# Kernel optimization log

Measured on AMD Instinct MI355X. Metric: run time of the kernel, lower is better.

Reference implementation:

```python
import jax, jax.numpy as jnp
import numpy as np
import math

THETA = 10000.0

def _rope(x, pos):
    # x: [B, H, S, Dh], pos: [S]
    d = x.shape[-1]
    inv_freq = 1.0 / (THETA ** (jnp.arange(0, d, 2, dtype=jnp.float32) / d))  # [Dh/2]
    ang = pos.astype(jnp.float32)[:, None] * inv_freq[None, :]                # [S, Dh/2]
    cos, sin = jnp.cos(ang), jnp.sin(ang)
    x1, x2 = x[..., 0::2], x[..., 1::2]
    r1 = x1 * cos - x2 * sin
    r2 = x1 * sin + x2 * cos
    return jnp.stack([r1, r2], axis=-1).reshape(x.shape)

def setup_inputs() -> dict:
    key = jax.random.key(0)
    ks = jax.random.split(key, 5)
    B, S, D = 2, 1024, 2048
    Dkv = 512
    scale = 1.0 / math.sqrt(D)
    return {
        "X": jax.random.normal(ks[0], (B, S, D), dtype=jnp.float32),
        "token_positions": jnp.arange(S, dtype=jnp.int32),
        "q_w": jax.random.normal(ks[1], (D, D), dtype=jnp.float32) * scale,
        "k_w": jax.random.normal(ks[2], (Dkv, D), dtype=jnp.float32) * scale,
        "v_w": jax.random.normal(ks[3], (Dkv, D), dtype=jnp.float32) * scale,
        "o_w": jax.random.normal(ks[4], (D, D), dtype=jnp.float32) * scale,
    }

def reference(X, token_positions, q_w, k_w, v_w, o_w):
    B, S, D = X.shape
    H, Hkv = 32, 8
    Dh = D // H
    G = H // Hkv  # query heads per KV head

    Q = (X @ q_w.T).reshape(B, S, H, Dh).transpose(0, 2, 1, 3)      # [B,H,S,Dh]
    K = (X @ k_w.T).reshape(B, S, Hkv, Dh).transpose(0, 2, 1, 3)    # [B,Hkv,S,Dh]
    V = (X @ v_w.T).reshape(B, S, Hkv, Dh).transpose(0, 2, 1, 3)    # [B,Hkv,S,Dh]

    Q = _rope(Q, token_positions)
    K = _rope(K, token_positions)

    # group query heads: [B, Hkv, G, S, Dh]
    Qg = Q.reshape(B, Hkv, G, S, Dh)
    scores = jnp.einsum('bkgqd,bkld->bkgql', Qg, K) / math.sqrt(Dh)  # [B,Hkv,G,S,S]
    causal = jnp.tril(jnp.ones((S, S), dtype=bool))
    scores = jnp.where(causal, scores, -jnp.inf)
    probs = jax.nn.softmax(scores, axis=-1)
    attn = jnp.einsum('bkgql,bkld->bkgqd', probs, V)                 # [B,Hkv,G,S,Dh]

    attn = attn.reshape(B, H, S, Dh).transpose(0, 2, 1, 3).reshape(B, S, D)
    return attn @ o_w.T
```

## Files before the change

### kernel.cpp

```cpp
#include <hip/hip_runtime.h>

typedef _Float16 f16;
typedef _Float16 half8 __attribute__((ext_vector_type(8), may_alias));
typedef _Float16 half4 __attribute__((ext_vector_type(4), may_alias));
typedef float f32x4 __attribute__((ext_vector_type(4), may_alias));

#define ROPE_KF -0.41524101186092027f
#define QSCALE 0.18033688011112042f

__device__ __forceinline__ void gload_lds16(const f16* g, f16* lds) {
  __builtin_amdgcn_global_load_lds(
      (const __attribute__((address_space(1))) void*)g,
      (__attribute__((address_space(3))) void*)lds, 16, 0, 0);
}

template <int N>
__device__ __forceinline__ void vm_wait() {
  if constexpr (N == 0) asm volatile("s_waitcnt vmcnt(0)" ::: "memory");
  else if constexpr (N == 3) asm volatile("s_waitcnt vmcnt(3)" ::: "memory");
  else if constexpr (N == 4) asm volatile("s_waitcnt vmcnt(4)" ::: "memory");
}

__device__ __forceinline__ half8 rope8s(half8 va, half8 vb, float posf, int i0,
                                        float scale) {
  half8 r;
#pragma unroll
  for (int p = 0; p < 4; ++p) {
    const float ang = posf * exp2f(ROPE_KF * (float)(i0 + p));
    float s, c;
    sincosf(ang, &s, &c);
    const float x1 = (float)va[2 * p] + (float)vb[2 * p];
    const float x2 = (float)va[2 * p + 1] + (float)vb[2 * p + 1];
    r[2 * p]     = (f16)((x1 * c - x2 * s) * scale);
    r[2 * p + 1] = (f16)((x1 * s + x2 * c) * scale);
  }
  return r;
}

__global__ __launch_bounds__(256) void cvt_all(const float* __restrict__ s0, f16* __restrict__ d0, int n0,
                                               const float* __restrict__ s1, f16* __restrict__ d1, int n1,
                                               const float* __restrict__ s2, f16* __restrict__ d2, int n2,
                                               const float* __restrict__ s3, f16* __restrict__ d3, int n3,
                                               const float* __restrict__ s4, f16* __restrict__ d4, int n4) {
  const int step = gridDim.x * blockDim.x * 4;
  const int base = (blockIdx.x * blockDim.x + threadIdx.x) * 4;
  auto go = [&](const float* s, f16* d, int n) {
    for (int i = base; i < n; i += step) {
      float4 v = *(const float4*)(s + i);
      half4 h;
      h[0] = (f16)v.x; h[1] = (f16)v.y; h[2] = (f16)v.z; h[3] = (f16)v.w;
      *(half4*)(d + i) = h;
    }
  };
  go(s0, d0, n0); go(s1, d1, n1); go(s2, d2, n2); go(s3, d3, n3); go(s4, d4, n4);
}

template <int OUT_F32, int BM>
__global__ __launch_bounds__(256, 2) void gemm_bt(const f16* __restrict__ A,
                                                  const f16* __restrict__ B,
                                                  void* __restrict__ Cv,
                                                  int M, int N, int K) {
  constexpr int NJ = (BM == 128) ? 4 : 2;
  constexpr int ACH = BM / 64;
  constexpr int LPS = ACH + 2;

  __shared__ alignas(16) f16 As[2][BM][32];
  __shared__ alignas(16) f16 Bs[2][128][32];
  const int tid = threadIdx.x;
  const int w = tid >> 6, l = tid & 63;
  const int m0 = blockIdx.y * BM, n0 = blockIdx.x << 7;
  const int klen = K / gridDim.z;
  const int koff = blockIdx.z * klen;
  const int fr = l & 15;
  const int fkz = (((l >> 4) ^ ((fr >> 1) & 3)) << 3);
  const int wr = (BM == 128) ? ((w >> 1) << 6) : 0;
  const int wc = (BM == 128) ? ((w & 1) << 6) : (w << 5);
  const int srow = l >> 2;
  const int scol = (((l & 3) ^ ((l >> 3) & 3)) << 3);

  const f16* ga = A + (size_t)(m0 + srow) * K + koff + scol;
  const f16* gb = B + (size_t)(n0 + srow) * K + koff + scol;

  auto stage = [&](int buf, int t) {
    const int k0 = t << 5;
#pragma unroll
    for (int c = 0; c < ACH; ++c) {
      const int rb = (w * ACH + c) << 4;
      gload_lds16(ga + (size_t)rb * K + k0, &As[buf][rb][0]);
    }
#pragma unroll
    for (int c = 0; c < 2; ++c) {
      const int rb = (w * 2 + c) << 4;
      gload_lds16(gb + (size_t)rb * K + k0, &Bs[buf][rb][0]);
    }
  };

  f32x4 acc[4][NJ] = {};

  stage(0, 0);
  stage(1, 1);
  const int nk = klen >> 5;
  for (int t = 0; t < nk; ++t) {
    const int buf = t & 1;
    if (t + 1 < nk) vm_wait<LPS>();
    else vm_wait<0>();
    __builtin_amdgcn_s_barrier();
    __builtin_amdgcn_sched_barrier(0);
    half8 af[4], bf[NJ];
#pragma unroll
    for (int i = 0; i < 4; ++i) af[i] = *(const half8*)&As[buf][wr + i * 16 + fr][fkz];
#pragma unroll
    for (int j = 0; j < NJ; ++j) bf[j] = *(const half8*)&Bs[buf][wc + j * 16 + fr][fkz];
#pragma unroll
    for (int i = 0; i < 4; ++i)
#pragma unroll
      for (int j = 0; j < NJ; ++j)
        acc[i][j] = __builtin_amdgcn_mfma_f32_16x16x32_f16(af[i], bf[j], acc[i][j], 0, 0, 0);
    __builtin_amdgcn_sched_barrier(0);
    __builtin_amdgcn_s_barrier();
    if (t + 2 < nk) stage(buf, t + 2);
  }

  const size_t zoff = (size_t)blockIdx.z * M * (size_t)N;
  const int orow = (l >> 4) << 2;
#pragma unroll
  for (int i = 0; i < 4; ++i) {
#pragma unroll
    for (int j = 0; j < NJ; ++j) {
      const int col = n0 + wc + j * 16 + fr;
#pragma unroll
      for (int r = 0; r < 4; ++r) {
        const size_t idx = zoff + (size_t)(m0 + wr + i * 16 + orow + r) * N + col;
        if (OUT_F32) ((float*)Cv)[idx] = acc[i][j][r];
        else ((f16*)Cv)[idx] = (f16)acc[i][j][r];
      }
    }
  }
}

__global__ __launch_bounds__(256) void repack_kv(const f16* __restrict__ QKV0,
                                                 const f16* __restrict__ QKV1,
                                                 const int* __restrict__ pos,
                                                 f16* __restrict__ Kp,
                                                 f16* __restrict__ Vt) {
  const int kt = blockIdx.x, kvh = blockIdx.y, b = blockIdx.z;
  const int tid = threadIdx.x;
  __shared__ f16 vs[64][72];
  const size_t tile = ((size_t)((b * 8 + kvh) * 16 + kt)) * 4096;
  const size_t kcol = 2048 + kvh * 64, vcol = 2560 + kvh * 64;
#pragma unroll
  for (int p = 0; p < 2; ++p) {
    const int c = tid + p * 256;
    const int row = c >> 3, slot = c & 7;
    const size_t grow = (size_t)(b * 1024 + kt * 64 + row) * 3072 + slot * 8;
    const half8 k0 = *(const half8*)(QKV0 + grow + kcol);
    const half8 k1 = *(const half8*)(QKV1 + grow + kcol);
    const half8 kk = rope8s(k0, k1, (float)pos[kt * 64 + row], slot << 2, 1.0f);
    *(half8*)(Kp + tile + row * 64 + ((slot ^ (row & 7)) << 3)) = kk;
    const half8 v0 = *(const half8*)(QKV0 + grow + vcol);
    const half8 v1 = *(const half8*)(QKV1 + grow + vcol);
    half8 vv;
#pragma unroll
    for (int ii = 0; ii < 8; ++ii) vv[ii] = (f16)((float)v0[ii] + (float)v1[ii]);
    *(half8*)&vs[row][slot * 8] = vv;
  }
  __syncthreads();
#pragma unroll
  for (int p = 0; p < 2; ++p) {
    const int c = tid + p * 256;
    const int d = c >> 3, oct = c & 7;
    half8 vv;
#pragma unroll
    for (int m = 0; m < 8; ++m) vv[m] = vs[oct * 8 + m][d];
    *(half8*)(Vt + tile + d * 64 + ((oct ^ (d & 7)) << 3)) = vv;
  }
}

__global__ __launch_bounds__(256) void attn_fwd(const f16* __restrict__ QKV0,
                                                const f16* __restrict__ QKV1,
                                                const f16* __restrict__ Kp,
                                                const f16* __restrict__ Vt,
                                                const int* __restrict__ pos,
                                                f16* __restrict__ O) {
  const int flat = blockIdx.x + (blockIdx.y << 3) + (blockIdx.z << 8);
  const int rmid = ((flat & 7) << 6) + (flat >> 3);
  const int pr = rmid & 7, h = (rmid >> 3) & 31, b = rmid >> 8;
  const int kvh = h >> 2;
  const int tid = threadIdx.x, w = tid >> 6, l = tid & 63;
  const int fr = l & 15, g = l >> 4;
  const int orow = g << 2;
  const int qtA = pr, qtB = 15 - pr;

  __shared__ alignas(16) char KsB[2][8192];
  __shared__ alignas(16) char VtB[2][8192];
  __shared__ alignas(16) f16 Ps[4][16][72];

  auto KS = [&](int buf, int row, int slot) -> f16* {
    return (f16*)(KsB[buf] + row * 128 + ((slot ^ (row & 7)) << 4));
  };
  auto VT = [&](int buf, int d, int oct) -> f16* {
    return (f16*)(VtB[buf] + d * 128 + ((oct ^ (d & 7)) << 4));
  };

  const int sA = qtA * 64 + w * 16 + fr, sB = qtB * 64 + w * 16 + fr;
  const float pA = (float)pos[sA], pB = (float)pos[sB];
  const size_t qoff = (size_t)(b * 1024 + w * 16 + fr) * 3072 + h * 64 + (g << 3);
  const size_t qoA = qoff + (size_t)qtA * 64 * 3072;
  const size_t qoB = qoff + (size_t)qtB * 64 * 3072;
  const half8 aA0 = rope8s(*(const half8*)(QKV0 + qoA), *(const half8*)(QKV1 + qoA),
                           pA, g << 2, QSCALE);
  const half8 aA1 = rope8s(*(const half8*)(QKV0 + qoA + 32), *(const half8*)(QKV1 + qoA + 32),
                           pA, 16 + (g << 2), QSCALE);
  const half8 aB0 = rope8s(*(const half8*)(QKV0 + qoB), *(const half8*)(QKV1 + qoB),
                           pB, g << 2, QSCALE);
  const half8 aB1 = rope8s(*(const half8*)(QKV0 + qoB + 32), *(const half8*)(QKV1 + qoB + 32),
                           pB, 16 + (g << 2), QSCALE);

  float rlA[4] = {0.f, 0.f, 0.f, 0.f}, rlB[4] = {0.f, 0.f, 0.f, 0.f};
  f32x4 oA[4] = {}, oB[4] = {};

  const size_t tbase = ((size_t)((b * 8 + kvh) * 16)) * 4096;
  const f16* kp0 = Kp + tbase + w * 1024 + (l << 3);
  const f16* vp0 = Vt + tbase + w * 1024 + (l << 3);
  auto stage = [&](int buf, int kt) {
    const f16* kp = kp0 + (size_t)kt * 4096;
    const f16* vp = vp0 + (size_t)kt * 4096;
    f16* kl = (f16*)(KsB[buf] + w * 2048);
    f16* vl = (f16*)(VtB[buf] + w * 2048);
    gload_lds16(kp, kl);
    gload_lds16(kp + 512, kl + 512);
    gload_lds16(vp, vl);
    gload_lds16(vp + 512, vl + 512);
  };

  auto compute = [&](int buf, const half8& a0, const half8& a1, float* rl,
                     f32x4* o, int qt, int kt) {
    f32x4 s4[4] = {};
#pragma unroll
    for (int j = 0; j < 4; ++j) {
      const half8 bk0 = *(const half8*)KS(buf, j * 16 + fr, g);
      const half8 bk1 = *(const half8*)KS(buf, j * 16 + fr, 4 + g);
      s4[j] = __builtin_amdgcn_mfma_f32_16x16x32_f16(a0, bk0, s4[j], 0, 0, 0);
      s4[j] = __builtin_amdgcn_mfma_f32_16x16x32_f16(a1, bk1, s4[j], 0, 0, 0);
    }
    if (kt == qt) {
      const int qrow0 = qt * 64 + w * 16 + orow;
#pragma unroll
      for (int j = 0; j < 4; ++j) {
        const int col = kt * 64 + j * 16 + fr;
#pragma unroll
        for (int r = 0; r < 4; ++r)
          if (col > qrow0 + r) s4[j][r] = -1.0e30f;
      }
    }
    float ps[4] = {0.f, 0.f, 0.f, 0.f};
#pragma unroll
    for (int j = 0; j < 4; ++j)
#pragma unroll
      for (int r = 0; r < 4; ++r) {
        const float p = exp2f(s4[j][r]);
        ps[r] += p;
        Ps[w][orow + r][j * 16 + fr] = (f16)p;
      }
#pragma unroll
    for (int r = 0; r < 4; ++r) rl[r] += ps[r];
#pragma unroll
    for (int kv2 = 0; kv2 < 2; ++kv2) {
      const half8 ap = *(const half8*)&Ps[w][fr][kv2 * 32 + (g << 3)];
#pragma unroll
      for (int j = 0; j < 4; ++j) {
        const half8 bv = *(const half8*)VT(buf, j * 16 + fr, kv2 * 4 + g);
        o[j] = __builtin_amdgcn_mfma_f32_16x16x32_f16(ap, bv, o[j], 0, 0, 0);
      }
    }
  };

  stage(0, 0);
  stage(1, 1);
  for (int kt = 0; kt <= qtB; ++kt) {
    const int buf = kt & 1;
    if (kt < qtB) vm_wait<4>();
    else vm_wait<0>();
    __builtin_amdgcn_s_barrier();
    __builtin_amdgcn_sched_barrier(0);
    if (kt <= qtA) compute(buf, aA0, aA1, rlA, oA, qtA, kt);
    compute(buf, aB0, aB1, rlB, oB, qtB, kt);
    __builtin_amdgcn_sched_barrier(0);
    __builtin_amdgcn_s_barrier();
    if (kt + 2 <= qtB) stage(buf, kt + 2);
  }

#pragma unroll
  for (int r = 0; r < 4; ++r) {
#pragma unroll
    for (int off = 8; off >= 1; off >>= 1) {
      rlA[r] += __shfl_xor(rlA[r], off);
      rlB[r] += __shfl_xor(rlB[r], off);
    }
  }

#pragma unroll
  for (int j = 0; j < 4; ++j)
#pragma unroll
    for (int r = 0; r < 4; ++r) {
      const int rowA = qtA * 64 + w * 16 + orow + r;
      const int rowB = qtB * 64 + w * 16 + orow + r;
      const int col = h * 64 + j * 16 + fr;
      O[(size_t)(b * 1024 + rowA) * 2048 + col] = (f16)(oA[j][r] / rlA[r]);
      O[(size_t)(b * 1024 + rowB) * 2048 + col] = (f16)(oB[j][r] / rlB[r]);
    }
}

extern "C" void kernel_launch(void* const* d_in, const int* in_sizes, int n_in,
                              void* d_out, int out_size, void* d_ws, size_t ws_size,
                              hipStream_t stream) {
  const float* X = (const float*)d_in[0];
  const int* tokpos = (const int*)d_in[1];
  const float* qw = (const float*)d_in[2];
  const float* kw = (const float*)d_in[3];
  const float* vw = (const float*)d_in[4];
  const float* ow = (const float*)d_in[5];

  constexpr int B = 2, S = 1024, D = 2048, DKV = 512, H = 32;
  constexpr int M = B * S;
  constexpr int NQKV = D + 2 * DKV;

  char* ws = (char*)d_ws;
  f16* Xh    = (f16*)(ws);
  f16* QKVW  = (f16*)(ws + (8u << 20));
  f16* owh   = (f16*)(ws + (20u << 20));
  f16* QKVc0 = (f16*)(ws + (28u << 20));
  f16* QKVc1 = (f16*)(ws + (40u << 20));
  f16* Kp    = (f16*)(ws);
  f16* Vt    = (f16*)(ws + (2u << 20));
  f16* Ah    = (f16*)(ws + (4u << 20));

  cvt_all<<<2048, 256, 0, stream>>>(X, Xh, M * D,
                                    qw, QKVW, D * D,
                                    kw, QKVW + (size_t)D * D, DKV * D,
                                    vw, QKVW + (size_t)(D + DKV) * D, DKV * D,
                                    ow, owh, D * D);

  gemm_bt<0, 128><<<dim3(NQKV / 128, M / 128, 2), 256, 0, stream>>>(Xh, QKVW, QKVc0,
                                                                    M, NQKV, D);

  repack_kv<<<dim3(16, 8, 2), 256, 0, stream>>>(QKVc0, QKVc1, tokpos, Kp, Vt);

  attn_fwd<<<dim3(8, H, B), 256, 0, stream>>>(QKVc0, QKVc1, Kp, Vt, tokpos, Ah);

  gemm_bt<1, 64><<<dim3(D / 128, M / 64, 1), 256, 0, stream>>>(Ah, owh, d_out, M, D, D);
}
```

Before: 121.4 us.

## Halve attention query tile per block and split-K the output projection

The attention kernel now runs 128-thread blocks over 32-row query tiles, each paired with its causal mirror, which doubles the block count to 1024. Each of the two waves loads twice as many K/V chunks per stage. The output projection switches to the 128-row split-K GEMM that writes two fp16 partial buffers, and a new reduce_out kernel sums them into fp32. The aim is better occupancy and load balance on the GPU. The cost is an extra kernel launch, an extra memory round trip, and partial sums rounded to fp16 before the final add.

```diff
diff --git a/kernel.cpp b/kernel.cpp
--- a/kernel.cpp
+++ b/kernel.cpp
@@ -19,6 +19,7 @@
   if constexpr (N == 0) asm volatile("s_waitcnt vmcnt(0)" ::: "memory");
   else if constexpr (N == 3) asm volatile("s_waitcnt vmcnt(3)" ::: "memory");
   else if constexpr (N == 4) asm volatile("s_waitcnt vmcnt(4)" ::: "memory");
+  else if constexpr (N == 8) asm volatile("s_waitcnt vmcnt(8)" ::: "memory");
 }
 
 __device__ __forceinline__ half8 rope8s(half8 va, half8 vb, float posf, int i0,
@@ -55,6 +56,23 @@
   go(s0, d0, n0); go(s1, d1, n1); go(s2, d2, n2); go(s3, d3, n3); go(s4, d4, n4);
 }
 
+__global__ __launch_bounds__(256) void reduce_out(const f16* __restrict__ a,
+                                                  const f16* __restrict__ b,
+                                                  float* __restrict__ o, int n) {
+  const int step = gridDim.x * blockDim.x * 8;
+  for (int i = (blockIdx.x * blockDim.x + threadIdx.x) * 8; i < n; i += step) {
+    const half8 va = *(const half8*)(a + i);
+    const half8 vb = *(const half8*)(b + i);
+    float4 o0, o1;
+    o0.x = (float)va[0] + (float)vb[0]; o0.y = (float)va[1] + (float)vb[1];
+    o0.z = (float)va[2] + (float)vb[2]; o0.w = (float)va[3] + (float)vb[3];
+    o1.x = (float)va[4] + (float)vb[4]; o1.y = (float)va[5] + (float)vb[5];
+    o1.z = (float)va[6] + (float)vb[6]; o1.w = (float)va[7] + (float)vb[7];
+    *(float4*)(o + i) = o0;
+    *(float4*)(o + i + 4) = o1;
+  }
+}
+
 template <int OUT_F32, int BM>
 __global__ __launch_bounds__(256, 2) void gemm_bt(const f16* __restrict__ A,
                                                   const f16* __restrict__ B,
@@ -176,24 +194,25 @@
   }
 }
 
-__global__ __launch_bounds__(256) void attn_fwd(const f16* __restrict__ QKV0,
+__global__ __launch_bounds__(128) void attn_fwd(const f16* __restrict__ QKV0,
                                                 const f16* __restrict__ QKV1,
                                                 const f16* __restrict__ Kp,
                                                 const f16* __restrict__ Vt,
                                                 const int* __restrict__ pos,
                                                 f16* __restrict__ O) {
-  const int flat = blockIdx.x + (blockIdx.y << 3) + (blockIdx.z << 8);
-  const int rmid = ((flat & 7) << 6) + (flat >> 3);
-  const int pr = rmid & 7, h = (rmid >> 3) & 31, b = rmid >> 8;
+  const int flat = blockIdx.x + (blockIdx.y << 4) + (blockIdx.z << 9);
+  const int rmid = ((flat & 7) << 7) + (flat >> 3);
+  const int pr = rmid & 15, h = (rmid >> 4) & 31, b = rmid >> 9;
   const int kvh = h >> 2;
   const int tid = threadIdx.x, w = tid >> 6, l = tid & 63;
   const int fr = l & 15, g = l >> 4;
   const int orow = g << 2;
-  const int qtA = pr, qtB = 15 - pr;
+  const int qtA = pr, qtB = 31 - pr;
+  const int ktA = qtA >> 1, ktB = qtB >> 1;
 
   __shared__ alignas(16) char KsB[2][8192];
   __shared__ alignas(16) char VtB[2][8192];
-  __shared__ alignas(16) f16 Ps[4][16][72];
+  __shared__ alignas(16) f16 Ps[2][16][72];
 
   auto KS = [&](int buf, int row, int slot) -> f16* {
     return (f16*)(KsB[buf] + row * 128 + ((slot ^ (row & 7)) << 4));
@@ -202,11 +221,11 @@
     return (f16*)(VtB[buf] + d * 128 + ((oct ^ (d & 7)) << 4));
   };
 
-  const int sA = qtA * 64 + w * 16 + fr, sB = qtB * 64 + w * 16 + fr;
+  const int sA = qtA * 32 + w * 16 + fr, sB = qtB * 32 + w * 16 + fr;
   const float pA = (float)pos[sA], pB = (float)pos[sB];
   const size_t qoff = (size_t)(b * 1024 + w * 16 + fr) * 3072 + h * 64 + (g << 3);
-  const size_t qoA = qoff + (size_t)qtA * 64 * 3072;
-  const size_t qoB = qoff + (size_t)qtB * 64 * 3072;
+  const size_t qoA = qoff + (size_t)qtA * 32 * 3072;
+  const size_t qoB = qoff + (size_t)qtB * 32 * 3072;
   const half8 aA0 = rope8s(*(const half8*)(QKV0 + qoA), *(const half8*)(QKV1 + qoA),
                            pA, g << 2, QSCALE);
   const half8 aA1 = rope8s(*(const half8*)(QKV0 + qoA + 32), *(const half8*)(QKV1 + qoA + 32),
@@ -220,17 +239,18 @@
   f32x4 oA[4] = {}, oB[4] = {};
 
   const size_t tbase = ((size_t)((b * 8 + kvh) * 16)) * 4096;
-  const f16* kp0 = Kp + tbase + w * 1024 + (l << 3);
-  const f16* vp0 = Vt + tbase + w * 1024 + (l << 3);
+  const f16* kp0 = Kp + tbase + w * 2048 + (l << 3);
+  const f16* vp0 = Vt + tbase + w * 2048 + (l << 3);
   auto stage = [&](int buf, int kt) {
     const f16* kp = kp0 + (size_t)kt * 4096;
     const f16* vp = vp0 + (size_t)kt * 4096;
-    f16* kl = (f16*)(KsB[buf] + w * 2048);
-    f16* vl = (f16*)(VtB[buf] + w * 2048);
-    gload_lds16(kp, kl);
-    gload_lds16(kp + 512, kl + 512);
-    gload_lds16(vp, vl);
-    gload_lds16(vp + 512, vl + 512);
+    f16* kl = (f16*)(KsB[buf] + w * 4096);
+    f16* vl = (f16*)(VtB[buf] + w * 4096);
+#pragma unroll
+    for (int c = 0; c < 4; ++c) {
+      gload_lds16(kp + c * 512, kl + c * 512);
+      gload_lds16(vp + c * 512, vl + c * 512);
+    }
   };
 
   auto compute = [&](int buf, const half8& a0, const half8& a1, float* rl,
@@ -243,8 +263,8 @@
       s4[j] = __builtin_amdgcn_mfma_f32_16x16x32_f16(a0, bk0, s4[j], 0, 0, 0);
       s4[j] = __builtin_amdgcn_mfma_f32_16x16x32_f16(a1, bk1, s4[j], 0, 0, 0);
     }
-    if (kt == qt) {
-      const int qrow0 = qt * 64 + w * 16 + orow;
+    if (kt == (qt >> 1)) {
+      const int qrow0 = qt * 32 + w * 16 + orow;
 #pragma unroll
       for (int j = 0; j < 4; ++j) {
         const int col = kt * 64 + j * 16 + fr;
@@ -277,17 +297,17 @@
 
   stage(0, 0);
   stage(1, 1);
-  for (int kt = 0; kt <= qtB; ++kt) {
+  for (int kt = 0; kt <= ktB; ++kt) {
     const int buf = kt & 1;
-    if (kt < qtB) vm_wait<4>();
+    if (kt < ktB) vm_wait<8>();
     else vm_wait<0>();
     __builtin_amdgcn_s_barrier();
     __builtin_amdgcn_sched_barrier(0);
-    if (kt <= qtA) compute(buf, aA0, aA1, rlA, oA, qtA, kt);
+    if (kt <= ktA) compute(buf, aA0, aA1, rlA, oA, qtA, kt);
     compute(buf, aB0, aB1, rlB, oB, qtB, kt);
     __builtin_amdgcn_sched_barrier(0);
     __builtin_amdgcn_s_barrier();
-    if (kt + 2 <= qtB) stage(buf, kt + 2);
+    if (kt + 2 <= ktB) stage(buf, kt + 2);
   }
 
 #pragma unroll
@@ -303,8 +323,8 @@
   for (int j = 0; j < 4; ++j)
 #pragma unroll
     for (int r = 0; r < 4; ++r) {
-      const int rowA = qtA * 64 + w * 16 + orow + r;
-      const int rowB = qtB * 64 + w * 16 + orow + r;
+      const int rowA = qtA * 32 + w * 16 + orow + r;
+      const int rowB = qtB * 32 + w * 16 + orow + r;
       const int col = h * 64 + j * 16 + fr;
       O[(size_t)(b * 1024 + rowA) * 2048 + col] = (f16)(oA[j][r] / rlA[r]);
       O[(size_t)(b * 1024 + rowB) * 2048 + col] = (f16)(oB[j][r] / rlB[r]);
@@ -334,6 +354,7 @@
   f16* Kp    = (f16*)(ws);
   f16* Vt    = (f16*)(ws + (2u << 20));
   f16* Ah    = (f16*)(ws + (4u << 20));
+  f16* Oh    = (f16*)(ws + (28u << 20));
 
   cvt_all<<<2048, 256, 0, stream>>>(X, Xh, M * D,
                                     qw, QKVW, D * D,
@@ -346,7 +367,9 @@
 
   repack_kv<<<dim3(16, 8, 2), 256, 0, stream>>>(QKVc0, QKVc1, tokpos, Kp, Vt);
 
-  attn_fwd<<<dim3(8, H, B), 256, 0, stream>>>(QKVc0, QKVc1, Kp, Vt, tokpos, Ah);
-
-  gemm_bt<1, 64><<<dim3(D / 128, M / 64, 1), 256, 0, stream>>>(Ah, owh, d_out, M, D, D);
-}
+  attn_fwd<<<dim3(16, H, B), 128, 0, stream>>>(QKVc0, QKVc1, Kp, Vt, tokpos, Ah);
+
+  gemm_bt<0, 128><<<dim3(D / 128, M / 128, 2), 256, 0, stream>>>(Ah, owh, Oh, M, D, D);
+
+  reduce_out<<<2048, 256, 0, stream>>>(Oh, Oh + (size_t)M * D, (float*)d_out, M * D);
+}
```

After: 124.4 us. 2.4% more time.
